# Performance work log

Measured on AMD Instinct MI355X. Metric: run time of the kernel, lower is better.

The kernel has to match this reference:

```python
import jax, jax.numpy as jnp
import numpy as np

D_MODEL = 1024
NUM_HEADS = 16
HEAD_DIM = D_MODEL // NUM_HEADS  # 64
THETA = 10000.0
B, S = 2, 2048


def setup_inputs() -> dict:
    key = jax.random.key(0)
    k1, k2, k3 = jax.random.split(key, 3)
    sigma_qkv = (2.0 / (D_MODEL + 3 * D_MODEL)) ** 0.5
    sigma_o = (2.0 / (D_MODEL + D_MODEL)) ** 0.5
    x = jax.random.normal(k1, (B, S, D_MODEL), dtype=jnp.float32)
    w_qkv = jax.random.normal(k2, (3 * D_MODEL, D_MODEL), dtype=jnp.float32) * sigma_qkv
    w_o = jax.random.normal(k3, (D_MODEL, D_MODEL), dtype=jnp.float32) * sigma_o
    token_positions = jnp.arange(S, dtype=jnp.int32)
    return {"x": x, "w_qkv": w_qkv, "w_o": w_o, "token_positions": token_positions, "mask": 1}


def _rope(t, pos):
    # t: (B, H, S, HEAD_DIM); pos: (S,) int
    ids = jnp.arange(HEAD_DIM // 2, dtype=jnp.float32)
    freqs = pos.astype(jnp.float32)[:, None] * (THETA ** (-2.0 * ids / HEAD_DIM))  # (S, HEAD_DIM/2)
    cos, sin = jnp.cos(freqs), jnp.sin(freqs)
    even, odd = t[..., 0::2], t[..., 1::2]
    r_even = even * cos - odd * sin
    r_odd = odd * cos + even * sin
    # interleave back to original layout
    return jnp.stack([r_even, r_odd], axis=-1).reshape(t.shape)


def reference(x, w_qkv, w_o, token_positions, mask):
    # fused QKV projection: Linear computes x @ W^T with W [out, in]
    qkv = x @ w_qkv.T  # (B, S, 3*D_MODEL)
    q, k, v = jnp.split(qkv, 3, axis=-1)

    def to_heads(t):
        return t.reshape(B, S, NUM_HEADS, HEAD_DIM).transpose(0, 2, 1, 3)  # (B, H, S, Dh)

    q, k, v = to_heads(q), to_heads(k), to_heads(v)
    q = _rope(q, token_positions)
    k = _rope(k, token_positions)

    scores = jnp.einsum('bhqd,bhkd->bhqk', q, k)
    if mask:  # causal: lower-triangular allowed
        causal = jnp.tril(jnp.ones((S, S), dtype=bool))
        scores = jnp.where(causal, scores, -jnp.inf)
    attn = jax.nn.softmax(scores * (HEAD_DIM ** -0.5), axis=-1)
    out = jnp.einsum('bhqk,bhkd->bhqd', attn, v)  # (B, H, S, Dh)
    out = out.transpose(0, 2, 1, 3).reshape(B, S, D_MODEL)
    return out @ w_o.T
```

## Files before the change

### kernel.cpp

```cpp
#include <hip/hip_runtime.h>
#include <hip/hip_bf16.h>
#include <math.h>

typedef __bf16 bf16_t;
typedef __bf16 bf16x8 __attribute__((ext_vector_type(8)));
typedef __bf16 bf16x4 __attribute__((ext_vector_type(4)));
typedef float  f32x4  __attribute__((ext_vector_type(4)));
typedef float  f32x16 __attribute__((ext_vector_type(16)));

#define D_MODEL 1024
#define NH      16
#define HD      64
#define BATCH   2
#define SEQ     2048
#define MROWS   (BATCH*SEQ)
#define QKVN    (3*D_MODEL)
#define FA_PAD  72
#define SCALE_LOG2E 0.18033688011112042f

__device__ __forceinline__ void async_cp16(const bf16_t* g, bf16_t* l) {
    __builtin_amdgcn_global_load_lds(
        (const __attribute__((address_space(1))) void*)g,
        (__attribute__((address_space(3))) void*)l,
        16, 0, 0);
}

__device__ __forceinline__ float fexp2(float x) {
    float r;
    asm("v_exp_f32 %0, %1" : "=v"(r) : "v"(x));
    return r;
}

__device__ __forceinline__ unsigned cvtpk(float lo, float hi_) {
    unsigned r;
    asm("v_cvt_pk_bf16_f32 %0, %1, %2" : "=v"(r) : "v"(lo), "v"(hi_));
    return r;
}

__global__ void cvt_all(const float* __restrict__ x, const float* __restrict__ wq,
                        const float* __restrict__ wo,
                        bf16_t* __restrict__ xb, bf16_t* __restrict__ wqb,
                        bf16_t* __restrict__ wob) {
    const int nx = MROWS * D_MODEL, nq = QKVN * D_MODEL;
    int i = (blockIdx.x * blockDim.x + threadIdx.x) * 4;
    const float* s; bf16_t* d; int off;
    if (i < nx)           { s = x;  d = xb;  off = i; }
    else if (i < nx + nq) { s = wq; d = wqb; off = i - nx; }
    else                  { s = wo; d = wob; off = i - nx - nq; }
    float4 v = *(const float4*)(s + off);
    d[off]     = (bf16_t)v.x;
    d[off + 1] = (bf16_t)v.y;
    d[off + 2] = (bf16_t)v.z;
    d[off + 3] = (bf16_t)v.w;
}

template <typename OutT, int NI>
__global__ __launch_bounds__(256) void gemm_nt(const bf16_t* __restrict__ A,
                                               const bf16_t* __restrict__ Bm,
                                               OutT* __restrict__ C,
                                               int M, int N, int K) {
    __shared__ __align__(16) bf16_t As[128 * 32];
    __shared__ __align__(16) bf16_t Bs[NI * 32 * 32];
    const int tid  = threadIdx.x;
    const int w    = tid >> 6;
    const int lane = tid & 63;
    const int quad = lane >> 4;
    const int l16  = lane & 15;
    const int m0   = blockIdx.x * 128;
    const int n0   = blockIdx.y * (NI * 32);
    const int wm   = (w >> 1) * 64;
    const int wn   = (w & 1) * (NI * 16);

    f32x4 acc[4][NI];
    #pragma unroll
    for (int i = 0; i < 4; i++)
        #pragma unroll
        for (int j = 0; j < NI; j++)
            acc[i][j] = (f32x4){0.f, 0.f, 0.f, 0.f};

    const bf16_t* Ag0 = A  + (size_t)(m0 + (tid >> 2)) * K + (tid & 3) * 8;
    const bf16_t* Ag1 = Ag0 + (size_t)64 * K;
    const bf16_t* Bg0 = Bm + (size_t)(n0 + (tid >> 2)) * K + (tid & 3) * 8;
    const bf16_t* Bg1 = Bg0 + (size_t)64 * K;
    bf16_t* Al0 = &As[(size_t)tid * 8];
    bf16_t* Al1 = &As[((size_t)tid + 256) * 8];
    bf16_t* Bl0 = &Bs[(size_t)tid * 8];
    bf16_t* Bl1 = &Bs[((size_t)tid + 256) * 8];

    for (int k0 = 0; k0 < K; k0 += 32) {
        async_cp16(Ag0 + k0, Al0);
        async_cp16(Ag1 + k0, Al1);
        async_cp16(Bg0 + k0, Bl0);
        if (NI == 4) async_cp16(Bg1 + k0, Bl1);
        __syncthreads();

        bf16x8 af[4], bfr[NI];
        #pragma unroll
        for (int mi = 0; mi < 4; mi++)
            af[mi] = *(const bf16x8*)&As[(wm + mi * 16 + l16) * 32 + quad * 8];
        #pragma unroll
        for (int ni = 0; ni < NI; ni++)
            bfr[ni] = *(const bf16x8*)&Bs[(wn + ni * 16 + l16) * 32 + quad * 8];
        #pragma unroll
        for (int mi = 0; mi < 4; mi++)
            #pragma unroll
            for (int ni = 0; ni < NI; ni++)
                acc[mi][ni] = __builtin_amdgcn_mfma_f32_16x16x32_bf16(
                    af[mi], bfr[ni], acc[mi][ni], 0, 0, 0);
        __syncthreads();
    }

    #pragma unroll
    for (int mi = 0; mi < 4; mi++)
        #pragma unroll
        for (int ni = 0; ni < NI; ni++) {
            const int col = n0 + wn + ni * 16 + l16;
            #pragma unroll
            for (int r = 0; r < 4; r++) {
                const int row = m0 + wm + mi * 16 + quad * 4 + r;
                C[(size_t)row * N + col] = (OutT)acc[mi][ni][r];
            }
        }
}

__global__ __launch_bounds__(256) void rope_split(const bf16_t* __restrict__ qkv,
                                                  const int* __restrict__ pos,
                                                  bf16_t* __restrict__ Qh,
                                                  bf16_t* __restrict__ Kh,
                                                  bf16_t* __restrict__ VT) {
    __shared__ bf16_t vs[128][FA_PAD];
    const int tid   = threadIdx.x;
    const int s_loc = tid >> 1;
    const int half  = tid & 1;
    const int s0    = blockIdx.x * 128;
    const int bh    = blockIdx.y;
    const int b     = bh >> 4, h = bh & 15;
    const int s     = s0 + s_loc;

    const bf16_t* row = qkv + (size_t)(b * SEQ + s) * QKVN + h * HD + half * 32;

    bf16_t qbuf[32], kbuf[32], vbuf[32];
    #pragma unroll
    for (int j = 0; j < 4; j++) {
        *(bf16x8*)&qbuf[j * 8] = *(const bf16x8*)(row + j * 8);
        *(bf16x8*)&kbuf[j * 8] = *(const bf16x8*)(row + D_MODEL + j * 8);
        *(bf16x8*)&vbuf[j * 8] = *(const bf16x8*)(row + 2 * D_MODEL + j * 8);
    }

    const float pf = (float)pos[s];
    #pragma unroll
    for (int p = 0; p < 16; p++) {
        const int d2 = half * 16 + p;
        const float inv = __expf(-0.28782313662425575f * (float)d2);
        const float f = pf * inv;
        const float c = cosf(f), sn = sinf(f);
        float qe = (float)qbuf[2 * p], qo = (float)qbuf[2 * p + 1];
        float ke = (float)kbuf[2 * p], ko = (float)kbuf[2 * p + 1];
        qbuf[2 * p]     = (bf16_t)((qe * c - qo * sn) * SCALE_LOG2E);
        qbuf[2 * p + 1] = (bf16_t)((qo * c + qe * sn) * SCALE_LOG2E);
        kbuf[2 * p]     = (bf16_t)(ke * c - ko * sn);
        kbuf[2 * p + 1] = (bf16_t)(ko * c + ke * sn);
    }

    bf16_t* qdst = Qh + ((size_t)bh * SEQ + s) * HD + half * 32;
    bf16_t* kdst = Kh + ((size_t)bh * SEQ + s) * HD + half * 32;
    #pragma unroll
    for (int j = 0; j < 4; j++) {
        *(bf16x8*)(qdst + j * 8) = *(bf16x8*)&qbuf[j * 8];
        *(bf16x8*)(kdst + j * 8) = *(bf16x8*)&kbuf[j * 8];
        *(bf16x8*)&vs[s_loc][half * 32 + j * 8] = *(bf16x8*)&vbuf[j * 8];
    }
    __syncthreads();

    const int d  = tid >> 2;
    const int sc = tid & 3;
    bf16_t tmp[32];
    #pragma unroll
    for (int i = 0; i < 32; i++) tmp[i] = vs[sc * 32 + i][d];
    bf16_t* vdst = VT + ((size_t)bh * HD + d) * SEQ + s0 + sc * 32;
    #pragma unroll
    for (int j = 0; j < 4; j++)
        *(bf16x8*)(vdst + j * 8) = *(bf16x8*)&tmp[j * 8];
}

__global__ __launch_bounds__(256) void flash_attn(const bf16_t* __restrict__ Qh,
                                                  const bf16_t* __restrict__ Kh,
                                                  const bf16_t* __restrict__ VT,
                                                  bf16_t* __restrict__ AO) {
    __shared__ __align__(16) bf16_t smem[4 * 64 * FA_PAD];
    bf16_t* Ks0 = smem;
    bf16_t* Vs0 = smem + 2 * 64 * FA_PAD;
    const int BUF = 64 * FA_PAD;

    const int tid  = threadIdx.x;
    const int w    = tid >> 6;
    const int lane = tid & 63;
    const int l31  = lane & 31;
    const int hi   = lane >> 5;
    const int qh   = w & 1;
    const int kh   = w >> 1;

    const int bid  = blockIdx.x;
    const int bh   = bid & 31;
    const int my_t = 31 - (bid >> 5);
    const int nkv  = my_t + 1;

    const bf16_t* Qb = Qh + (size_t)bh * SEQ * HD;
    const bf16_t* Kb = Kh + (size_t)bh * SEQ * HD;
    const bf16_t* Vb = VT + (size_t)bh * HD * SEQ;

    const int q0b = my_t * 64;
    const int qlo = q0b + qh * 32;
    const int qg  = qlo + l31;

    bf16x8 aq[4];
    #pragma unroll
    for (int ks = 0; ks < 4; ks++)
        aq[ks] = *(const bf16x8*)(Qb + (size_t)qg * HD + ks * 16 + hi * 8);

    const int srow = tid >> 3, scol = (tid & 7) * 8;
    const int lds0 = srow * FA_PAD + scol;
    const int lds1 = (srow + 32) * FA_PAD + scol;

    f32x16 o[2];
    #pragma unroll
    for (int dt = 0; dt < 2; dt++)
        #pragma unroll
        for (int i = 0; i < 16; i++) o[dt][i] = 0.f;
    float ls = 0.f;

    bf16x8 pK0 = *(const bf16x8*)(Kb + (size_t)srow * HD + scol);
    bf16x8 pK1 = *(const bf16x8*)(Kb + (size_t)(srow + 32) * HD + scol);
    bf16x8 pV0 = *(const bf16x8*)(Vb + (size_t)srow * SEQ + scol);
    bf16x8 pV1 = *(const bf16x8*)(Vb + (size_t)(srow + 32) * SEQ + scol);
    *(bf16x8*)&Ks0[lds0] = pK0;
    *(bf16x8*)&Ks0[lds1] = pK1;
    *(bf16x8*)&Vs0[lds0] = pV0;
    *(bf16x8*)&Vs0[lds1] = pV1;

    for (int kt = 0; kt < nkv; ++kt) {
        const int cur = kt & 1;
        __syncthreads();

        if (kt + 1 < nkv) {
            const int kn = (kt + 1) * 64;
            pK0 = *(const bf16x8*)(Kb + (size_t)(kn + srow) * HD + scol);
            pK1 = *(const bf16x8*)(Kb + (size_t)(kn + srow + 32) * HD + scol);
            pV0 = *(const bf16x8*)(Vb + (size_t)srow * SEQ + kn + scol);
            pV1 = *(const bf16x8*)(Vb + (size_t)(srow + 32) * SEQ + kn + scol);
        }

        const bf16_t* KsC = Ks0 + cur * BUF;
        const bf16_t* VsC = Vs0 + cur * BUF;
        const int kvbw = kt * 64 + kh * 32;
        if (kvbw <= qlo + 31) {
            const bool full = (kvbw + 31 <= qlo);

            bf16x8 kb[4];
            #pragma unroll
            for (int ks = 0; ks < 4; ks++)
                kb[ks] = *(const bf16x8*)&KsC[(kh * 32 + l31) * FA_PAD + ks * 16 + hi * 8];
            f32x16 t;
            #pragma unroll
            for (int i = 0; i < 16; i++) t[i] = 0.f;
            #pragma unroll
            for (int ks = 0; ks < 4; ks++)
                t = __builtin_amdgcn_mfma_f32_32x32x16_bf16(kb[ks], aq[ks], t, 0, 0, 0);

            float pv[16];
            #pragma unroll
            for (int r = 0; r < 16; r++) {
                float p = fexp2(t[r]);
                if (!full) {
                    const int kvg = kvbw + (r & 3) + 8 * (r >> 2) + 4 * hi;
                    if (kvg > qg) p = 0.f;
                }
                pv[r] = p;
            }
            ls += ((((pv[0] + pv[1]) + (pv[2] + pv[3]))
                  + ((pv[4] + pv[5]) + (pv[6] + pv[7])))
                 + (((pv[8] + pv[9]) + (pv[10] + pv[11]))
                  + ((pv[12] + pv[13]) + (pv[14] + pv[15]))));

            union { unsigned u[4]; bf16x8 v; } pa0, pa1;
            {
                unsigned a0 = cvtpk(pv[0], pv[1]);
                unsigned b0 = cvtpk(pv[4], pv[5]);
                unsigned a1 = cvtpk(pv[2], pv[3]);
                unsigned b1 = cvtpk(pv[6], pv[7]);
                asm volatile("v_permlane32_swap_b32 %0, %1" : "+v"(a0), "+v"(b0));
                asm volatile("v_permlane32_swap_b32 %0, %1" : "+v"(a1), "+v"(b1));
                pa0.u[0] = a0; pa0.u[1] = a1; pa0.u[2] = b0; pa0.u[3] = b1;
            }
            {
                unsigned a0 = cvtpk(pv[8], pv[9]);
                unsigned b0 = cvtpk(pv[12], pv[13]);
                unsigned a1 = cvtpk(pv[10], pv[11]);
                unsigned b1 = cvtpk(pv[14], pv[15]);
                asm volatile("v_permlane32_swap_b32 %0, %1" : "+v"(a0), "+v"(b0));
                asm volatile("v_permlane32_swap_b32 %0, %1" : "+v"(a1), "+v"(b1));
                pa1.u[0] = a0; pa1.u[1] = a1; pa1.u[2] = b0; pa1.u[3] = b1;
            }

            #pragma unroll
            for (int dt = 0; dt < 2; dt++) {
                const int vbase = (dt * 32 + l31) * FA_PAD + kh * 32 + hi * 8;
                bf16x8 vf0 = *(const bf16x8*)&VsC[vbase];
                bf16x8 vf1 = *(const bf16x8*)&VsC[vbase + 16];
                o[dt] = __builtin_amdgcn_mfma_f32_32x32x16_bf16(pa0.v, vf0, o[dt], 0, 0, 0);
                o[dt] = __builtin_amdgcn_mfma_f32_32x32x16_bf16(pa1.v, vf1, o[dt], 0, 0, 0);
            }
        }

        if (kt + 1 < nkv) {
            bf16_t* KsN = Ks0 + (cur ^ 1) * BUF;
            bf16_t* VsN = Vs0 + (cur ^ 1) * BUF;
            *(bf16x8*)&KsN[lds0] = pK0;
            *(bf16x8*)&KsN[lds1] = pK1;
            *(bf16x8*)&VsN[lds0] = pV0;
            *(bf16x8*)&VsN[lds1] = pV1;
        }
    }

    __syncthreads();
    ls += __shfl_xor(ls, 32);
    float* mrgO = (float*)smem;
    float* lsp  = mrgO + 2 * 32 * 66;
    if (kh == 1) {
        #pragma unroll
        for (int r = 0; r < 16; r++) {
            const int qlc = (r & 3) + 8 * (r >> 2) + 4 * hi;
            #pragma unroll
            for (int dt = 0; dt < 2; dt++)
                mrgO[(qh * 32 + qlc) * 66 + dt * 32 + l31] = o[dt][r];
        }
        if (hi == 0) lsp[qh * 32 + l31] = ls;
    }
    __syncthreads();
    if (kh == 0) {
        const float lt = ls + lsp[qh * 32 + l31];
        const int b = bh >> 4, hh = bh & 15;
        #pragma unroll
        for (int r = 0; r < 16; r++) {
            const int qlc = (r & 3) + 8 * (r >> 2) + 4 * hi;
            const float li = 1.0f / __shfl(lt, qlc);
            const size_t row = (size_t)b * SEQ + q0b + qh * 32 + qlc;
            #pragma unroll
            for (int dt = 0; dt < 2; dt++) {
                const float v = o[dt][r] + mrgO[(qh * 32 + qlc) * 66 + dt * 32 + l31];
                AO[row * D_MODEL + hh * HD + dt * 32 + l31] = (bf16_t)(v * li);
            }
        }
    }
}

extern "C" void kernel_launch(void* const* d_in, const int* in_sizes, int n_in,
                              void* d_out, int out_size, void* d_ws, size_t ws_size,
                              hipStream_t stream) {
    const float* x     = (const float*)d_in[0];
    const float* w_qkv = (const float*)d_in[1];
    const float* w_o   = (const float*)d_in[2];
    const int*   tpos  = (const int*)d_in[3];
    float*       out   = (float*)d_out;

    char* ws = (char*)d_ws;
    bf16_t* xb  = (bf16_t*)(ws);
    bf16_t* wqb = (bf16_t*)(ws + 8388608);
    bf16_t* wob = (bf16_t*)(ws + 14680064);
    bf16_t* qkv = (bf16_t*)(ws + 16777216);
    bf16_t* Qh  = (bf16_t*)(ws + 41943040);
    bf16_t* Kh  = (bf16_t*)(ws + 50331648);
    bf16_t* VT  = (bf16_t*)(ws + 58720256);
    bf16_t* AO  = (bf16_t*)(ws + 67108864);

    cvt_all<<<8192, 256, 0, stream>>>(x, w_qkv, w_o, xb, wqb, wob);

    gemm_nt<bf16_t, 4><<<dim3(32, 24), 256, 0, stream>>>(xb, wqb, qkv, MROWS, QKVN, D_MODEL);

    rope_split<<<dim3(SEQ / 128, BATCH * NH), 256, 0, stream>>>(qkv, tpos, Qh, Kh, VT);

    flash_attn<<<1024, 256, 0, stream>>>(Qh, Kh, VT, AO);

    gemm_nt<float, 2><<<dim3(32, 16), 256, 0, stream>>>(AO, wob, out, MROWS, D_MODEL, D_MODEL);
}
```

Before: 192.2 us.

## Pair complementary causal query tiles per block to share K/V loads

Each flash-attention block now handles two query tiles, tile 31-u and tile u. Every block therefore does the same total causal work, and each K/V tile staged in LDS serves both query tiles. The grid is halved and the LDS merge buffer is doubled to hold both tiles' partial outputs and row sums. The cost is higher register pressure from two sets of Q fragments and accumulators, plus fewer blocks in flight, which may lower occupancy.

```diff
diff --git a/kernel.cpp b/kernel.cpp
--- a/kernel.cpp
+++ b/kernel.cpp
@@ -202,32 +202,35 @@
 
     const int bid  = blockIdx.x;
     const int bh   = bid & 31;
-    const int my_t = 31 - (bid >> 5);
-    const int nkv  = my_t + 1;
+    const int u    = bid >> 5;
+    const int tA   = 31 - u;
+    const int tB   = u;
+    const int nkv  = tA + 1;
 
     const bf16_t* Qb = Qh + (size_t)bh * SEQ * HD;
     const bf16_t* Kb = Kh + (size_t)bh * SEQ * HD;
     const bf16_t* Vb = VT + (size_t)bh * HD * SEQ;
 
-    const int q0b = my_t * 64;
-    const int qlo = q0b + qh * 32;
-    const int qg  = qlo + l31;
-
-    bf16x8 aq[4];
-    #pragma unroll
-    for (int ks = 0; ks < 4; ks++)
-        aq[ks] = *(const bf16x8*)(Qb + (size_t)qg * HD + ks * 16 + hi * 8);
+    const int qloA = tA * 64 + qh * 32, qgA = qloA + l31;
+    const int qloB = tB * 64 + qh * 32, qgB = qloB + l31;
+
+    bf16x8 aqA[4], aqB[4];
+    #pragma unroll
+    for (int ks = 0; ks < 4; ks++) {
+        aqA[ks] = *(const bf16x8*)(Qb + (size_t)qgA * HD + ks * 16 + hi * 8);
+        aqB[ks] = *(const bf16x8*)(Qb + (size_t)qgB * HD + ks * 16 + hi * 8);
+    }
 
     const int srow = tid >> 3, scol = (tid & 7) * 8;
     const int lds0 = srow * FA_PAD + scol;
     const int lds1 = (srow + 32) * FA_PAD + scol;
 
-    f32x16 o[2];
+    f32x16 oA[2], oB[2];
     #pragma unroll
     for (int dt = 0; dt < 2; dt++)
         #pragma unroll
-        for (int i = 0; i < 16; i++) o[dt][i] = 0.f;
-    float ls = 0.f;
+        for (int i = 0; i < 16; i++) { oA[dt][i] = 0.f; oB[dt][i] = 0.f; }
+    float lsA = 0.f, lsB = 0.f;
 
     bf16x8 pK0 = *(const bf16x8*)(Kb + (size_t)srow * HD + scol);
     bf16x8 pK1 = *(const bf16x8*)(Kb + (size_t)(srow + 32) * HD + scol);
@@ -238,6 +241,53 @@
     *(bf16x8*)&Vs0[lds0] = pV0;
     *(bf16x8*)&Vs0[lds1] = pV1;
 
+#define QUAD(AQ, QG, O, LS, FULL) {                                            \
+    f32x16 t;                                                                  \
+    _Pragma("unroll")                                                          \
+    for (int i = 0; i < 16; i++) t[i] = 0.f;                                   \
+    _Pragma("unroll")                                                          \
+    for (int ks = 0; ks < 4; ks++)                                             \
+        t = __builtin_amdgcn_mfma_f32_32x32x16_bf16(kb[ks], AQ[ks], t, 0, 0, 0); \
+    float pv[16];                                                              \
+    _Pragma("unroll")                                                          \
+    for (int r = 0; r < 16; r++) {                                             \
+        float p = fexp2(t[r]);                                                 \
+        if (!(FULL)) {                                                         \
+            const int kvg = kvbw + (r & 3) + 8 * (r >> 2) + 4 * hi;            \
+            if (kvg > (QG)) p = 0.f;                                           \
+        }                                                                      \
+        pv[r] = p;                                                             \
+    }                                                                          \
+    LS += ((((pv[0] + pv[1]) + (pv[2] + pv[3]))                                \
+          + ((pv[4] + pv[5]) + (pv[6] + pv[7])))                               \
+         + (((pv[8] + pv[9]) + (pv[10] + pv[11]))                              \
+          + ((pv[12] + pv[13]) + (pv[14] + pv[15]))));                         \
+    union { unsigned uu[4]; bf16x8 v; } pa0, pa1;                              \
+    {                                                                          \
+        unsigned a0 = cvtpk(pv[0], pv[1]);                                     \
+        unsigned b0 = cvtpk(pv[4], pv[5]);                                     \
+        unsigned a1 = cvtpk(pv[2], pv[3]);                                     \
+        unsigned b1 = cvtpk(pv[6], pv[7]);                                     \
+        asm volatile("v_permlane32_swap_b32 %0, %1" : "+v"(a0), "+v"(b0));     \
+        asm volatile("v_permlane32_swap_b32 %0, %1" : "+v"(a1), "+v"(b1));     \
+        pa0.uu[0] = a0; pa0.uu[1] = a1; pa0.uu[2] = b0; pa0.uu[3] = b1;        \
+    }                                                                          \
+    {                                                                          \
+        unsigned a0 = cvtpk(pv[8], pv[9]);                                     \
+        unsigned b0 = cvtpk(pv[12], pv[13]);                                   \
+        unsigned a1 = cvtpk(pv[10], pv[11]);                                   \
+        unsigned b1 = cvtpk(pv[14], pv[15]);                                   \
+        asm volatile("v_permlane32_swap_b32 %0, %1" : "+v"(a0), "+v"(b0));     \
+        asm volatile("v_permlane32_swap_b32 %0, %1" : "+v"(a1), "+v"(b1));     \
+        pa1.uu[0] = a0; pa1.uu[1] = a1; pa1.uu[2] = b0; pa1.uu[3] = b1;        \
+    }                                                                          \
+    _Pragma("unroll")                                                          \
+    for (int dt = 0; dt < 2; dt++) {                                           \
+        O[dt] = __builtin_amdgcn_mfma_f32_32x32x16_bf16(pa0.v, vfr[dt][0], O[dt], 0, 0, 0); \
+        O[dt] = __builtin_amdgcn_mfma_f32_32x32x16_bf16(pa1.v, vfr[dt][1], O[dt], 0, 0, 0); \
+    }                                                                          \
+}
+
     for (int kt = 0; kt < nkv; ++kt) {
         const int cur = kt & 1;
         __syncthreads();
@@ -253,62 +303,28 @@
         const bf16_t* KsC = Ks0 + cur * BUF;
         const bf16_t* VsC = Vs0 + cur * BUF;
         const int kvbw = kt * 64 + kh * 32;
-        if (kvbw <= qlo + 31) {
-            const bool full = (kvbw + 31 <= qlo);
-
+        const bool actA = (kvbw <= qloA + 31);
+        const bool actB = (kt <= tB) && (kvbw <= qloB + 31);
+
+        if (actA || actB) {
             bf16x8 kb[4];
             #pragma unroll
             for (int ks = 0; ks < 4; ks++)
                 kb[ks] = *(const bf16x8*)&KsC[(kh * 32 + l31) * FA_PAD + ks * 16 + hi * 8];
-            f32x16 t;
-            #pragma unroll
-            for (int i = 0; i < 16; i++) t[i] = 0.f;
-            #pragma unroll
-            for (int ks = 0; ks < 4; ks++)
-                t = __builtin_amdgcn_mfma_f32_32x32x16_bf16(kb[ks], aq[ks], t, 0, 0, 0);
-
-            float pv[16];
-            #pragma unroll
-            for (int r = 0; r < 16; r++) {
-                float p = fexp2(t[r]);
-                if (!full) {
-                    const int kvg = kvbw + (r & 3) + 8 * (r >> 2) + 4 * hi;
-                    if (kvg > qg) p = 0.f;
-                }
-                pv[r] = p;
-            }
-            ls += ((((pv[0] + pv[1]) + (pv[2] + pv[3]))
-                  + ((pv[4] + pv[5]) + (pv[6] + pv[7])))
-                 + (((pv[8] + pv[9]) + (pv[10] + pv[11]))
-                  + ((pv[12] + pv[13]) + (pv[14] + pv[15]))));
-
-            union { unsigned u[4]; bf16x8 v; } pa0, pa1;
-            {
-                unsigned a0 = cvtpk(pv[0], pv[1]);
-                unsigned b0 = cvtpk(pv[4], pv[5]);
-                unsigned a1 = cvtpk(pv[2], pv[3]);
-                unsigned b1 = cvtpk(pv[6], pv[7]);
-                asm volatile("v_permlane32_swap_b32 %0, %1" : "+v"(a0), "+v"(b0));
-                asm volatile("v_permlane32_swap_b32 %0, %1" : "+v"(a1), "+v"(b1));
-                pa0.u[0] = a0; pa0.u[1] = a1; pa0.u[2] = b0; pa0.u[3] = b1;
-            }
-            {
-                unsigned a0 = cvtpk(pv[8], pv[9]);
-                unsigned b0 = cvtpk(pv[12], pv[13]);
-                unsigned a1 = cvtpk(pv[10], pv[11]);
-                unsigned b1 = cvtpk(pv[14], pv[15]);
-                asm volatile("v_permlane32_swap_b32 %0, %1" : "+v"(a0), "+v"(b0));
-                asm volatile("v_permlane32_swap_b32 %0, %1" : "+v"(a1), "+v"(b1));
-                pa1.u[0] = a0; pa1.u[1] = a1; pa1.u[2] = b0; pa1.u[3] = b1;
-            }
-
+            bf16x8 vfr[2][2];
             #pragma unroll
             for (int dt = 0; dt < 2; dt++) {
                 const int vbase = (dt * 32 + l31) * FA_PAD + kh * 32 + hi * 8;
-                bf16x8 vf0 = *(const bf16x8*)&VsC[vbase];
-                bf16x8 vf1 = *(const bf16x8*)&VsC[vbase + 16];
-                o[dt] = __builtin_amdgcn_mfma_f32_32x32x16_bf16(pa0.v, vf0, o[dt], 0, 0, 0);
-                o[dt] = __builtin_amdgcn_mfma_f32_32x32x16_bf16(pa1.v, vf1, o[dt], 0, 0, 0);
+                vfr[dt][0] = *(const bf16x8*)&VsC[vbase];
+                vfr[dt][1] = *(const bf16x8*)&VsC[vbase + 16];
+            }
+            if (actA) {
+                const bool fullA = (kvbw + 31 <= qloA);
+                QUAD(aqA, qgA, oA, lsA, fullA);
+            }
+            if (actB) {
+                const bool fullB = (kvbw + 31 <= qloB);
+                QUAD(aqB, qgB, oB, lsB, fullB);
             }
         }
 
@@ -321,34 +337,46 @@
             *(bf16x8*)&VsN[lds1] = pV1;
         }
     }
+#undef QUAD
 
     __syncthreads();
-    ls += __shfl_xor(ls, 32);
+    lsA += __shfl_xor(lsA, 32);
+    lsB += __shfl_xor(lsB, 32);
     float* mrgO = (float*)smem;
-    float* lsp  = mrgO + 2 * 32 * 66;
+    float* lsp  = mrgO + 4 * 32 * 66;
     if (kh == 1) {
         #pragma unroll
         for (int r = 0; r < 16; r++) {
             const int qlc = (r & 3) + 8 * (r >> 2) + 4 * hi;
             #pragma unroll
-            for (int dt = 0; dt < 2; dt++)
-                mrgO[(qh * 32 + qlc) * 66 + dt * 32 + l31] = o[dt][r];
-        }
-        if (hi == 0) lsp[qh * 32 + l31] = ls;
+            for (int dt = 0; dt < 2; dt++) {
+                mrgO[((0 * 2 + qh) * 32 + qlc) * 66 + dt * 32 + l31] = oA[dt][r];
+                mrgO[((1 * 2 + qh) * 32 + qlc) * 66 + dt * 32 + l31] = oB[dt][r];
+            }
+        }
+        if (hi == 0) {
+            lsp[0 * 64 + qh * 32 + l31] = lsA;
+            lsp[1 * 64 + qh * 32 + l31] = lsB;
+        }
     }
     __syncthreads();
     if (kh == 0) {
-        const float lt = ls + lsp[qh * 32 + l31];
         const int b = bh >> 4, hh = bh & 15;
+        const float ltA = lsA + lsp[0 * 64 + qh * 32 + l31];
+        const float ltB = lsB + lsp[1 * 64 + qh * 32 + l31];
         #pragma unroll
         for (int r = 0; r < 16; r++) {
             const int qlc = (r & 3) + 8 * (r >> 2) + 4 * hi;
-            const float li = 1.0f / __shfl(lt, qlc);
-            const size_t row = (size_t)b * SEQ + q0b + qh * 32 + qlc;
+            const float liA = 1.0f / __shfl(ltA, qlc);
+            const float liB = 1.0f / __shfl(ltB, qlc);
+            const size_t rowA = (size_t)b * SEQ + tA * 64 + qh * 32 + qlc;
+            const size_t rowB = (size_t)b * SEQ + tB * 64 + qh * 32 + qlc;
             #pragma unroll
             for (int dt = 0; dt < 2; dt++) {
-                const float v = o[dt][r] + mrgO[(qh * 32 + qlc) * 66 + dt * 32 + l31];
-                AO[row * D_MODEL + hh * HD + dt * 32 + l31] = (bf16_t)(v * li);
+                const float vA = oA[dt][r] + mrgO[((0 * 2 + qh) * 32 + qlc) * 66 + dt * 32 + l31];
+                const float vB = oB[dt][r] + mrgO[((1 * 2 + qh) * 32 + qlc) * 66 + dt * 32 + l31];
+                AO[rowA * D_MODEL + hh * HD + dt * 32 + l31] = (bf16_t)(vA * liA);
+                AO[rowB * D_MODEL + hh * HD + dt * 32 + l31] = (bf16_t)(vB * liB);
             }
         }
     }
@@ -379,7 +407,7 @@
 
     rope_split<<<dim3(SEQ / 128, BATCH * NH), 256, 0, stream>>>(qkv, tpos, Qh, Kh, VT);
 
-    flash_attn<<<1024, 256, 0, stream>>>(Qh, Kh, VT, AO);
+    flash_attn<<<512, 256, 0, stream>>>(Qh, Kh, VT, AO);
 
     gemm_nt<float, 2><<<dim3(32, 16), 256, 0, stream>>>(AO, wob, out, MROWS, D_MODEL, D_MODEL);
 }
```

After: 196.6 us. 2.3% more time.
